# Optimization experiments

Hardware: AMD Instinct MI355X
Metric: run time of the kernel (lower is better)

Reference implementation:

```python
import jax, jax.numpy as jnp
import numpy as np

B, N, M = 262144, 8, 8      # batch, state dim, control dim (n_vars == n_controls)
H1, H21, H22 = 64, 32, 32
R2 = 16.0                   # barrier h(x) = R2 - ||x||^2
UMIN, UMAX = -1.0, 1.0


def setup_inputs() -> dict:
    key = jax.random.key(0)
    ks = jax.random.split(key, 12)
    init = lambda k, sh: jax.random.normal(k, sh, jnp.float32) / np.float32(np.sqrt(sh[0]))
    return {
        "x":   jax.random.normal(ks[0], (B, N), jnp.float32),
        "W1":  init(ks[1], (N, H1)),   "b1":  jnp.zeros((H1,), jnp.float32),
        "W21": init(ks[2], (H1, H21)), "b21": jnp.zeros((H21,), jnp.float32),
        "W22": init(ks[3], (H1, H22)), "b22": jnp.zeros((H22,), jnp.float32),
        "W31": init(ks[4], (H21, M)),  "b31": jnp.zeros((M,), jnp.float32),
        "W32": init(ks[5], (H22, 1)),  "b32": jnp.zeros((1,), jnp.float32),
        "A":   0.1 * jax.random.normal(ks[6], (N, N), jnp.float32),  # f(x) = A x
        "G":   init(ks[7], (N, M)),                                  # g(x) = G
        "mean": jnp.zeros((N,), jnp.float32),
        "std":  jnp.ones((N,), jnp.float32),
    }


def _qp_solve(p, g, c0):
    """Batched exact solution of: argmin_u 1/2||u||^2 + p.u
    s.t. UMIN <= u <= UMAX,  c0 + g . u >= 0   (one QP per row).
    KKT: u(lam) = clip(-p + lam*g, UMIN, UMAX), lam >= 0 dual of the CBF
    constraint; c(lam) = c0 + g.u(lam) is nondecreasing in lam, so lam* is
    found by bracketing + bisection, then refined in closed form on the
    frozen active set (this also yields exact implicit KKT derivatives)."""
    def c_of(lam):
        u = jnp.clip(-p + lam[:, None] * g, UMIN, UMAX)
        return c0 + jnp.sum(g * u, axis=-1)

    # bracket lambda* in [0, hi]
    hi = jax.lax.fori_loop(0, 40, lambda i, h: jnp.where(c_of(h) < 0, 2.0 * h, h),
                           jnp.ones_like(c0))

    def bis(i, lh):
        lo, hi = lh
        mid = 0.5 * (lo + hi)
        neg = c_of(mid) < 0
        return jnp.where(neg, mid, lo), jnp.where(neg, hi, mid)

    lo, hi = jax.lax.fori_loop(0, 60, bis, (jnp.zeros_like(c0), hi))
    lam_b = 0.5 * (lo + hi)

    # frozen active sets -> closed-form lambda consistent with KKT
    u_raw = -p + lam_b[:, None] * g
    low = jax.lax.stop_gradient(u_raw <= UMIN)
    high = jax.lax.stop_gradient(u_raw >= UMAX)
    free = ~(low | high)
    viol = jax.lax.stop_gradient(c_of(jnp.zeros_like(c0)) < 0)  # constraint active?
    denom = jnp.sum(jnp.where(free, g * g, 0.0), axis=-1)
    num = c0 + jnp.sum(jnp.where(low, UMIN * g, 0.0)
                       + jnp.where(high, UMAX * g, 0.0)
                       - jnp.where(free, g * p, 0.0), axis=-1)
    lam = jnp.where(viol, -num / (denom + 1e-12), 0.0)
    return jnp.where(low, UMIN, jnp.where(high, UMAX, -p + lam[:, None] * g))


def reference(x, W1, b1, W21, b21, W22, b22, W31, b31, W32, b32, A, G, mean, std):
    x0 = x * std + mean                                   # un-normalized state (B, N)
    h1 = jax.nn.relu(x @ W1 + b1)                         # (B, H1)
    x21 = jax.nn.relu(h1 @ W21 + b21)                     # (B, H21)
    x22 = jax.nn.relu(h1 @ W22 + b22)                     # (B, H22)
    px = x21 @ W31 + b31                                  # nominal control (B, M)
    alphax = 4.0 * jax.nn.sigmoid(x22 @ W32 + b32)        # class-K gain (B, 1)
    hx = R2 - jnp.sum(x0 * x0, axis=-1, keepdims=True)    # barrier value (B, 1)
    dhdx = -2.0 * x0                                      # barrier gradient (B, N)
    fxv = x0 @ A.T                                        # f(x) = A x        (B, N)
    Lfhx = jnp.sum(dhdx * fxv, axis=-1)                   # (B,)
    Lghx = dhdx @ G                                       # (B, M)
    c0 = Lfhx + (alphax * hx)[:, 0]                       # (B,)
    return _qp_solve(px, Lghx, c0)                        # safe control u (B, M)
```

## Files before the change

### kernel.cpp

```cpp
#include <hip/hip_runtime.h>

#define NN 8
#define MM 8
#define NH1 64
#define NH2 32

#define FOR8(OP) OP(0) OP(1) OP(2) OP(3) OP(4) OP(5) OP(6) OP(7)

typedef float v2f  __attribute__((ext_vector_type(2)));
typedef float sf16 __attribute__((ext_vector_type(16)));

#define S_ISSUE2(d0, d1, base, imm)                                    \
    asm volatile("s_load_dwordx16 %0, %2, %c3\n\t"                     \
                 "s_load_dwordx16 %1, %2, %c4"                         \
                 : "=&s"(d0), "=&s"(d1)                                \
                 : "s"(base), "n"(imm), "n"((imm) + 64))

#define S_ISSUE1(d0, base, imm)                                        \
    asm volatile("s_load_dwordx16 %0, %1, %c2"                         \
                 : "=&s"(d0) : "s"(base), "n"(imm))

#define S_WAIT2(d0, d1)                                                \
    asm volatile("s_waitcnt lgkmcnt(0)" : "+s"(d0), "+s"(d1))

#define S_WAIT1(d0)                                                    \
    asm volatile("s_waitcnt lgkmcnt(0)" : "+s"(d0))

#define PKFMA(acc, w, xi)                                              \
    asm("v_pk_fma_f32 %0, %1, %2, %0" : "+v"(acc) : "s"(w), "v"(xi))

__device__ __forceinline__ void compute_row(
    int row,
    const float* __restrict__ x_g,
    const float* __restrict__ W1,  const float* __restrict__ b1,
    const float* __restrict__ W21, const float* __restrict__ b21,
    const float* __restrict__ W22, const float* __restrict__ b22,
    const float* __restrict__ W31, const float* __restrict__ b31,
    const float* __restrict__ W32, const float* __restrict__ b32,
    const float* __restrict__ Amat, const float* __restrict__ Gmat,
    const float* __restrict__ mean, const float* __restrict__ std_,
    float* __restrict__ out)
{
    float x[NN];
    {
        const float4* xv = reinterpret_cast<const float4*>(x_g + (size_t)row * NN);
        float4 a0 = xv[0], a1 = xv[1];
        x[0] = a0.x; x[1] = a0.y; x[2] = a0.z; x[3] = a0.w;
        x[4] = a1.x; x[5] = a1.y; x[6] = a1.z; x[7] = a1.w;
    }

    float x0[NN];
    {
        const float4 sd0 = ((const float4*)std_)[0], sd1 = ((const float4*)std_)[1];
        const float4 mn0 = ((const float4*)mean)[0], mn1 = ((const float4*)mean)[1];
        x0[0] = fmaf(x[0], sd0.x, mn0.x); x0[1] = fmaf(x[1], sd0.y, mn0.y);
        x0[2] = fmaf(x[2], sd0.z, mn0.z); x0[3] = fmaf(x[3], sd0.w, mn0.w);
        x0[4] = fmaf(x[4], sd1.x, mn1.x); x0[5] = fmaf(x[5], sd1.y, mn1.y);
        x0[6] = fmaf(x[6], sd1.z, mn1.z); x0[7] = fmaf(x[7], sd1.w, mn1.w);
    }

    v2f hv[NH1 / 2];
#pragma unroll
    for (int j2 = 0; j2 < NH1 / 2; ++j2) hv[j2] = *(const v2f*)(b1 + 2 * j2);

    {
        sf16 rA0, rA1, rB0, rB1;
        S_ISSUE2(rA0, rA1, W1, 0);
        S_WAIT2(rA0, rA1);
#pragma unroll
        for (int u = 0; u < 16; ++u) {
            const int i = u >> 1, hh = u & 1;
            const v2f xi = { x[i], x[i] };
            if ((u & 1) == 0) {
                if (u + 1 < 16) S_ISSUE2(rB0, rB1, W1, (u + 1) * 128);
#pragma unroll
                for (int j2 = 0; j2 < 8; ++j2) { const v2f w = { rA0[2*j2], rA0[2*j2+1] }; PKFMA(hv[hh*16 + j2], w, xi); }
#pragma unroll
                for (int j2 = 0; j2 < 8; ++j2) { const v2f w = { rA1[2*j2], rA1[2*j2+1] }; PKFMA(hv[hh*16 + 8 + j2], w, xi); }
                if (u + 1 < 16) S_WAIT2(rB0, rB1);
            } else {
                if (u + 1 < 16) S_ISSUE2(rA0, rA1, W1, (u + 1) * 128);
#pragma unroll
                for (int j2 = 0; j2 < 8; ++j2) { const v2f w = { rB0[2*j2], rB0[2*j2+1] }; PKFMA(hv[hh*16 + j2], w, xi); }
#pragma unroll
                for (int j2 = 0; j2 < 8; ++j2) { const v2f w = { rB1[2*j2], rB1[2*j2+1] }; PKFMA(hv[hh*16 + 8 + j2], w, xi); }
                if (u + 1 < 16) S_WAIT2(rA0, rA1);
            }
        }
    }
    {
        const v2f zero2 = { 0.0f, 0.0f };
#pragma unroll
        for (int j2 = 0; j2 < NH1 / 2; ++j2) hv[j2] = __builtin_elementwise_max(hv[j2], zero2);
    }

    v2f a21[NH2 / 2], a22[NH2 / 2];
#pragma unroll
    for (int j2 = 0; j2 < NH2 / 2; ++j2) {
        a21[j2] = *(const v2f*)(b21 + 2 * j2);
        a22[j2] = *(const v2f*)(b22 + 2 * j2);
    }

#define L2PASS(ACC, WBASE)                                                     \
    {                                                                          \
        sf16 qA0, qA1, qB0, qB1;                                               \
        S_ISSUE2(qA0, qA1, WBASE, 0);                                          \
        S_WAIT2(qA0, qA1);                                                     \
        _Pragma("unroll")                                                      \
        for (int k = 0; k < NH1; ++k) {                                        \
            const v2f hb = (k & 1) ? hv[k >> 1].yy : hv[k >> 1].xx;            \
            if ((k & 1) == 0) {                                                \
                if (k + 1 < NH1) S_ISSUE2(qB0, qB1, WBASE, (k + 1) * 128);     \
                _Pragma("unroll")                                              \
                for (int j2 = 0; j2 < 8; ++j2) { const v2f w = { qA0[2*j2], qA0[2*j2+1] }; PKFMA(ACC[j2], w, hb); } \
                _Pragma("unroll")                                              \
                for (int j2 = 0; j2 < 8; ++j2) { const v2f w = { qA1[2*j2], qA1[2*j2+1] }; PKFMA(ACC[8 + j2], w, hb); } \
                if (k + 1 < NH1) S_WAIT2(qB0, qB1);                            \
            } else {                                                           \
                if (k + 1 < NH1) S_ISSUE2(qA0, qA1, WBASE, (k + 1) * 128);     \
                _Pragma("unroll")                                              \
                for (int j2 = 0; j2 < 8; ++j2) { const v2f w = { qB0[2*j2], qB0[2*j2+1] }; PKFMA(ACC[j2], w, hb); } \
                _Pragma("unroll")                                              \
                for (int j2 = 0; j2 < 8; ++j2) { const v2f w = { qB1[2*j2], qB1[2*j2+1] }; PKFMA(ACC[8 + j2], w, hb); } \
                if (k + 1 < NH1) S_WAIT2(qA0, qA1);                            \
            }                                                                  \
        }                                                                      \
    }

    L2PASS(a21, W21)
    L2PASS(a22, W22)
#undef L2PASS

    {
        const v2f zero2 = { 0.0f, 0.0f };
#pragma unroll
        for (int j2 = 0; j2 < NH2 / 2; ++j2) {
            a21[j2] = __builtin_elementwise_max(a21[j2], zero2);
            a22[j2] = __builtin_elementwise_max(a22[j2], zero2);
        }
    }

    sf16 wA0, wA1;
    S_ISSUE2(wA0, wA1, W32, 0);

    v2f pv[MM / 2];
#pragma unroll
    for (int j2 = 0; j2 < MM / 2; ++j2) pv[j2] = *(const v2f*)(b31 + 2 * j2);
    {
        sf16 pA, pB;
        S_ISSUE1(pA, W31, 0);
        S_WAIT1(pA);
#pragma unroll
        for (int k2 = 0; k2 < NH2 / 2; ++k2) {
            const v2f ha = a21[k2].xx, hb2 = a21[k2].yy;
            if ((k2 & 1) == 0) {
                if (k2 + 1 < 16) S_ISSUE1(pB, W31, (k2 + 1) * 64);
#pragma unroll
                for (int j2 = 0; j2 < 4; ++j2) { const v2f w = { pA[2*j2], pA[2*j2+1] }; PKFMA(pv[j2], w, ha); }
#pragma unroll
                for (int j2 = 0; j2 < 4; ++j2) { const v2f w = { pA[8 + 2*j2], pA[8 + 2*j2+1] }; PKFMA(pv[j2], w, hb2); }
                if (k2 + 1 < 16) S_WAIT1(pB);
            } else {
                if (k2 + 1 < 16) S_ISSUE1(pA, W31, (k2 + 1) * 64);
#pragma unroll
                for (int j2 = 0; j2 < 4; ++j2) { const v2f w = { pB[2*j2], pB[2*j2+1] }; PKFMA(pv[j2], w, ha); }
#pragma unroll
                for (int j2 = 0; j2 < 4; ++j2) { const v2f w = { pB[8 + 2*j2], pB[8 + 2*j2+1] }; PKFMA(pv[j2], w, hb2); }
                if (k2 + 1 < 16) S_WAIT1(pA);
            }
        }
    }

    S_WAIT2(wA0, wA1);
    float s = b32[0];
#pragma unroll
    for (int k = 0; k < 16; ++k)
        s = fmaf((k & 1) ? a22[k >> 1].y : a22[k >> 1].x, wA0[k], s);
#pragma unroll
    for (int k = 16; k < 32; ++k)
        s = fmaf((k & 1) ? a22[k >> 1].y : a22[k >> 1].x, wA1[k - 16], s);
    const float alphax = 4.0f / (1.0f + __expf(-s));

    float hx = 16.0f;
#pragma unroll
    for (int i = 0; i < NN; ++i) hx = fmaf(-x0[i], x0[i], hx);

    float dh[NN];
#pragma unroll
    for (int i = 0; i < NN; ++i) dh[i] = -2.0f * x0[i];

    float Lfhx = 0.0f;
#pragma unroll
    for (int i = 0; i < NN; ++i) {
        const float4 aq0 = *(const float4*)(Amat + i * NN);
        const float4 aq1 = *(const float4*)(Amat + i * NN + 4);
        float fx = 0.0f;
        fx = fmaf(aq0.x, x0[0], fx); fx = fmaf(aq0.y, x0[1], fx);
        fx = fmaf(aq0.z, x0[2], fx); fx = fmaf(aq0.w, x0[3], fx);
        fx = fmaf(aq1.x, x0[4], fx); fx = fmaf(aq1.y, x0[5], fx);
        fx = fmaf(aq1.z, x0[6], fx); fx = fmaf(aq1.w, x0[7], fx);
        Lfhx = fmaf(dh[i], fx, Lfhx);
    }

#define GDECL(j) float g##j = 0.0f;
    FOR8(GDECL)
#undef GDECL
#pragma unroll
    for (int i = 0; i < NN; ++i) {
        const float4 gq0 = *(const float4*)(Gmat + i * MM);
        const float4 gq1 = *(const float4*)(Gmat + i * MM + 4);
        const float da = dh[i];
        g0 = fmaf(da, gq0.x, g0); g1 = fmaf(da, gq0.y, g1);
        g2 = fmaf(da, gq0.z, g2); g3 = fmaf(da, gq0.w, g3);
        g4 = fmaf(da, gq1.x, g4); g5 = fmaf(da, gq1.y, g5);
        g6 = fmaf(da, gq1.z, g6); g7 = fmaf(da, gq1.w, g7);
    }

    const float c0 = fmaf(alphax, hx, Lfhx);

#define DECL_PG(j) const float p##j = (j & 1) ? pv[j >> 1].y : pv[j >> 1].x;
    FOR8(DECL_PG)
#undef DECL_PG

    auto c_of = [&](float lam) -> float {
        float c = c0;
#define CTERM(j) { float u = fmaf(lam, g##j, -p##j);                  \
                   u = fminf(fmaxf(u, -1.0f), 1.0f);                  \
                   c = fmaf(g##j, u, c); }
        FOR8(CTERM)
#undef CTERM
        return c;
    };

    const bool viol = (c_of(0.0f) < 0.0f);

    const float BIGR = 3.0e38f;
    float lamL = 0.0f, lamR = BIGR;
#define BP(j) {                                                        \
        const float rg = __builtin_amdgcn_rcpf(g##j);                  \
        const float bpa = (p##j - 1.0f) * rg;                          \
        const float bpb = (p##j + 1.0f) * rg;                          \
        const float ca = c_of(bpa);                                    \
        const float cb = c_of(bpb);                                    \
        lamL = (bpa > 0.0f && ca <  0.0f && bpa > lamL) ? bpa : lamL;  \
        lamR = (bpa > 0.0f && ca >= 0.0f && bpa < lamR) ? bpa : lamR;  \
        lamL = (bpb > 0.0f && cb <  0.0f && bpb > lamL) ? bpb : lamL;  \
        lamR = (bpb > 0.0f && cb >= 0.0f && bpb < lamR) ? bpb : lamR;  \
    }
    FOR8(BP)
#undef BP

    const bool infeas = (lamR == BIGR);
    float lam_t = infeas ? 1.099511627776e12f : 0.5f * (lamL + lamR);
    lam_t = viol ? lam_t : 0.0f;

    float denom = 0.0f, num = c0;
#define ASET(j)                                                        \
    const float ur##j = fmaf(lam_t, g##j, -p##j);                      \
    const bool lo##j = (ur##j <= -1.0f);                               \
    const bool hi##j = (ur##j >=  1.0f);                               \
    denom += (!(lo##j || hi##j)) ? g##j * g##j : 0.0f;                 \
    num   += lo##j ? -g##j : (hi##j ? g##j : -g##j * p##j);
    FOR8(ASET)
#undef ASET

    const float lam = viol ? (-num / (denom + 1e-12f)) : 0.0f;

#define UOUT(j) const float uo##j =                                    \
    lo##j ? -1.0f : (hi##j ? 1.0f : fmaf(lam, g##j, -p##j));
    FOR8(UOUT)
#undef UOUT

    float4* ov = reinterpret_cast<float4*>(out + (size_t)row * MM);
    ov[0] = make_float4(uo0, uo1, uo2, uo3);
    ov[1] = make_float4(uo4, uo5, uo6, uo7);
}

#define ARGS_DECL                                                       \
    const float* __restrict__ x_g,                                      \
    const float* __restrict__ W1,  const float* __restrict__ b1,        \
    const float* __restrict__ W21, const float* __restrict__ b21,       \
    const float* __restrict__ W22, const float* __restrict__ b22,       \
    const float* __restrict__ W31, const float* __restrict__ b31,       \
    const float* __restrict__ W32, const float* __restrict__ b32,       \
    const float* __restrict__ Amat, const float* __restrict__ Gmat,     \
    const float* __restrict__ mean, const float* __restrict__ std_,    \
    float* __restrict__ out
#define ARGS_PASS x_g, W1, b1, W21, b21, W22, b22, W31, b31, W32, b32, \
                  Amat, Gmat, mean, std_, out

__global__ __launch_bounds__(256, 2) void barrier_policy_clean(ARGS_DECL)
{
    const int row = blockIdx.x * 256 + threadIdx.x;
    compute_row(row, ARGS_PASS);
}

__global__ __launch_bounds__(256, 2) void barrier_policy_guard(ARGS_DECL, int B)
{
    const int row = blockIdx.x * 256 + threadIdx.x;
    if (row < B) compute_row(row, ARGS_PASS);
}

extern "C" void kernel_launch(void* const* d_in, const int* in_sizes, int n_in,
                              void* d_out, int out_size, void* d_ws, size_t ws_size,
                              hipStream_t stream) {
    const float* x    = (const float*)d_in[0];
    const float* W1   = (const float*)d_in[1];
    const float* b1   = (const float*)d_in[2];
    const float* W21  = (const float*)d_in[3];
    const float* b21  = (const float*)d_in[4];
    const float* W22  = (const float*)d_in[5];
    const float* b22  = (const float*)d_in[6];
    const float* W31  = (const float*)d_in[7];
    const float* b31  = (const float*)d_in[8];
    const float* W32  = (const float*)d_in[9];
    const float* b32  = (const float*)d_in[10];
    const float* Amat = (const float*)d_in[11];
    const float* Gmat = (const float*)d_in[12];
    const float* mean = (const float*)d_in[13];
    const float* std_ = (const float*)d_in[14];
    float* out = (float*)d_out;

    const int B = in_sizes[0] / NN;
    if (B % 256 == 0) {
        barrier_policy_clean<<<B / 256, 256, 0, stream>>>(
            x, W1, b1, W21, b21, W22, b22, W31, b31, W32, b32,
            Amat, Gmat, mean, std_, out);
    } else {
        barrier_policy_guard<<<(B + 255) / 256, 256, 0, stream>>>(
            x, W1, b1, W21, b21, W22, b22, W31, b31, W32, b32,
            Amat, Gmat, mean, std_, out, B);
    }
}
```

Measured before the change: 43.57 us.

## Compute W21 hidden layer with packed fp16 dot2 and raise occupancy bound

Adds a small prep kernel that converts W21 to packed fp16 pairs in the workspace. The main kernel packs the first hidden activations into fp16 and computes the second-layer x21 branch with v_dot2_f32_f16, which accumulates pairs along the reduction dimension in fp32. It also moves the alpha (sigmoid) computation earlier so the W32 load overlaps the ReLU, and changes launch_bounds from 2 to 4 waves per SIMD. This adds an extra launch, reduces precision of the nominal control feeding the QP, and the tighter register budget may cause spills.

```diff
diff --git a/kernel.cpp b/kernel.cpp
--- a/kernel.cpp
+++ b/kernel.cpp
@@ -1,4 +1,5 @@
 #include <hip/hip_runtime.h>
+#include <hip/hip_fp16.h>
 
 #define NN 8
 #define MM 8
@@ -9,6 +10,7 @@
 
 typedef float v2f  __attribute__((ext_vector_type(2)));
 typedef float sf16 __attribute__((ext_vector_type(16)));
+typedef __fp16 h2f __attribute__((ext_vector_type(2)));
 
 #define S_ISSUE2(d0, d1, base, imm)                                    \
     asm volatile("s_load_dwordx16 %0, %2, %c3\n\t"                     \
@@ -29,12 +31,27 @@
 #define PKFMA(acc, w, xi)                                              \
     asm("v_pk_fma_f32 %0, %1, %2, %0" : "+v"(acc) : "s"(w), "v"(xi))
 
+#define DOT2(acc, w, hp)                                               \
+    asm("v_dot2_f32_f16 %0, %2, %1, %0" : "+v"(acc) : "s"(w), "v"(hp))
+
+__global__ void prep_f16(const float* __restrict__ W21,
+                         unsigned int* __restrict__ ws)
+{
+    const int t = blockIdx.x * 256 + threadIdx.x;
+    const int k2 = t >> 5, j = t & 31;
+    const float lo = W21[(2 * k2) * NH2 + j];
+    const float hi = W21[(2 * k2 + 1) * NH2 + j];
+    const __half hlo = __float2half(lo), hhi = __float2half(hi);
+    ws[t] = ((unsigned int)__half_as_ushort(hhi) << 16) | __half_as_ushort(hlo);
+}
+
 __device__ __forceinline__ void compute_row(
     int row,
     const float* __restrict__ x_g,
     const float* __restrict__ W1,  const float* __restrict__ b1,
-    const float* __restrict__ W21, const float* __restrict__ b21,
-    const float* __restrict__ W22, const float* __restrict__ b22,
+    const float* __restrict__ ws21,
+    const float* __restrict__ b21, const float* __restrict__ b22,
+    const float* __restrict__ W22,
     const float* __restrict__ W31, const float* __restrict__ b31,
     const float* __restrict__ W32, const float* __restrict__ b32,
     const float* __restrict__ Amat, const float* __restrict__ Gmat,
@@ -94,54 +111,91 @@
         for (int j2 = 0; j2 < NH1 / 2; ++j2) hv[j2] = __builtin_elementwise_max(hv[j2], zero2);
     }
 
-    v2f a21[NH2 / 2], a22[NH2 / 2];
-#pragma unroll
-    for (int j2 = 0; j2 < NH2 / 2; ++j2) {
-        a21[j2] = *(const v2f*)(b21 + 2 * j2);
-        a22[j2] = *(const v2f*)(b22 + 2 * j2);
-    }
-
-#define L2PASS(ACC, WBASE)                                                     \
-    {                                                                          \
-        sf16 qA0, qA1, qB0, qB1;                                               \
-        S_ISSUE2(qA0, qA1, WBASE, 0);                                          \
-        S_WAIT2(qA0, qA1);                                                     \
-        _Pragma("unroll")                                                      \
-        for (int k = 0; k < NH1; ++k) {                                        \
-            const v2f hb = (k & 1) ? hv[k >> 1].yy : hv[k >> 1].xx;            \
-            if ((k & 1) == 0) {                                                \
-                if (k + 1 < NH1) S_ISSUE2(qB0, qB1, WBASE, (k + 1) * 128);     \
-                _Pragma("unroll")                                              \
-                for (int j2 = 0; j2 < 8; ++j2) { const v2f w = { qA0[2*j2], qA0[2*j2+1] }; PKFMA(ACC[j2], w, hb); } \
-                _Pragma("unroll")                                              \
-                for (int j2 = 0; j2 < 8; ++j2) { const v2f w = { qA1[2*j2], qA1[2*j2+1] }; PKFMA(ACC[8 + j2], w, hb); } \
-                if (k + 1 < NH1) S_WAIT2(qB0, qB1);                            \
-            } else {                                                           \
-                if (k + 1 < NH1) S_ISSUE2(qA0, qA1, WBASE, (k + 1) * 128);     \
-                _Pragma("unroll")                                              \
-                for (int j2 = 0; j2 < 8; ++j2) { const v2f w = { qB0[2*j2], qB0[2*j2+1] }; PKFMA(ACC[j2], w, hb); } \
-                _Pragma("unroll")                                              \
-                for (int j2 = 0; j2 < 8; ++j2) { const v2f w = { qB1[2*j2], qB1[2*j2+1] }; PKFMA(ACC[8 + j2], w, hb); } \
-                if (k + 1 < NH1) S_WAIT2(qA0, qA1);                            \
-            }                                                                  \
-        }                                                                      \
-    }
-
-    L2PASS(a21, W21)
-    L2PASS(a22, W22)
-#undef L2PASS
-
-    {
-        const v2f zero2 = { 0.0f, 0.0f };
-#pragma unroll
-        for (int j2 = 0; j2 < NH2 / 2; ++j2) {
-            a21[j2] = __builtin_elementwise_max(a21[j2], zero2);
-            a22[j2] = __builtin_elementwise_max(a22[j2], zero2);
+    v2f a22[NH2 / 2];
+#pragma unroll
+    for (int j2 = 0; j2 < NH2 / 2; ++j2) a22[j2] = *(const v2f*)(b22 + 2 * j2);
+    {
+        sf16 qA0, qA1, qB0, qB1;
+        S_ISSUE2(qA0, qA1, W22, 0);
+        S_WAIT2(qA0, qA1);
+#pragma unroll
+        for (int k = 0; k < NH1; ++k) {
+            const v2f hb = (k & 1) ? hv[k >> 1].yy : hv[k >> 1].xx;
+            if ((k & 1) == 0) {
+                if (k + 1 < NH1) S_ISSUE2(qB0, qB1, W22, (k + 1) * 128);
+#pragma unroll
+                for (int j2 = 0; j2 < 8; ++j2) { const v2f w = { qA0[2*j2], qA0[2*j2+1] }; PKFMA(a22[j2], w, hb); }
+#pragma unroll
+                for (int j2 = 0; j2 < 8; ++j2) { const v2f w = { qA1[2*j2], qA1[2*j2+1] }; PKFMA(a22[8 + j2], w, hb); }
+                if (k + 1 < NH1) S_WAIT2(qB0, qB1);
+            } else {
+                if (k + 1 < NH1) S_ISSUE2(qA0, qA1, W22, (k + 1) * 128);
+#pragma unroll
+                for (int j2 = 0; j2 < 8; ++j2) { const v2f w = { qB0[2*j2], qB0[2*j2+1] }; PKFMA(a22[j2], w, hb); }
+#pragma unroll
+                for (int j2 = 0; j2 < 8; ++j2) { const v2f w = { qB1[2*j2], qB1[2*j2+1] }; PKFMA(a22[8 + j2], w, hb); }
+                if (k + 1 < NH1) S_WAIT2(qA0, qA1);
+            }
         }
     }
 
     sf16 wA0, wA1;
     S_ISSUE2(wA0, wA1, W32, 0);
+    {
+        const v2f zero2 = { 0.0f, 0.0f };
+#pragma unroll
+        for (int j2 = 0; j2 < NH2 / 2; ++j2) a22[j2] = __builtin_elementwise_max(a22[j2], zero2);
+    }
+    S_WAIT2(wA0, wA1);
+    float s = b32[0];
+#pragma unroll
+    for (int k = 0; k < 16; ++k)
+        s = fmaf((k & 1) ? a22[k >> 1].y : a22[k >> 1].x, wA0[k], s);
+#pragma unroll
+    for (int k = 16; k < 32; ++k)
+        s = fmaf((k & 1) ? a22[k >> 1].y : a22[k >> 1].x, wA1[k - 16], s);
+    const float alphax = 4.0f / (1.0f + __expf(-s));
+
+    float hpk[NH1 / 2];
+#pragma unroll
+    for (int k2 = 0; k2 < NH1 / 2; ++k2) {
+        h2f hp = __builtin_amdgcn_cvt_pkrtz(hv[k2].x, hv[k2].y);
+        hpk[k2] = __builtin_bit_cast(float, hp);
+    }
+
+    float a21s[NH2];
+#pragma unroll
+    for (int j4 = 0; j4 < NH2 / 4; ++j4) {
+        const float4 i21 = ((const float4*)b21)[j4];
+        a21s[4*j4]   = i21.x; a21s[4*j4+1] = i21.y;
+        a21s[4*j4+2] = i21.z; a21s[4*j4+3] = i21.w;
+    }
+    {
+        sf16 A0, A1, B0, B1;
+        S_ISSUE2(A0, A1, ws21, 0);
+        S_WAIT2(A0, A1);
+#pragma unroll
+        for (int k2 = 0; k2 < 32; ++k2) {
+            const float hp = hpk[k2];
+            if ((k2 & 1) == 0) {
+                if (k2 + 1 < 32) S_ISSUE2(B0, B1, ws21, (k2 + 1) * 128);
+#pragma unroll
+                for (int j = 0; j < 16; ++j) DOT2(a21s[j],      A0[j], hp);
+#pragma unroll
+                for (int j = 0; j < 16; ++j) DOT2(a21s[16 + j], A1[j], hp);
+                if (k2 + 1 < 32) S_WAIT2(B0, B1);
+            } else {
+                if (k2 + 1 < 32) S_ISSUE2(A0, A1, ws21, (k2 + 1) * 128);
+#pragma unroll
+                for (int j = 0; j < 16; ++j) DOT2(a21s[j],      B0[j], hp);
+#pragma unroll
+                for (int j = 0; j < 16; ++j) DOT2(a21s[16 + j], B1[j], hp);
+                if (k2 + 1 < 32) S_WAIT2(A0, A1);
+            }
+        }
+    }
+#pragma unroll
+    for (int j = 0; j < NH2; ++j) a21s[j] = fmaxf(a21s[j], 0.0f);
 
     v2f pv[MM / 2];
 #pragma unroll
@@ -152,7 +206,8 @@
         S_WAIT1(pA);
 #pragma unroll
         for (int k2 = 0; k2 < NH2 / 2; ++k2) {
-            const v2f ha = a21[k2].xx, hb2 = a21[k2].yy;
+            const v2f ha  = { a21s[2*k2],     a21s[2*k2]     };
+            const v2f hb2 = { a21s[2*k2 + 1], a21s[2*k2 + 1] };
             if ((k2 & 1) == 0) {
                 if (k2 + 1 < 16) S_ISSUE1(pB, W31, (k2 + 1) * 64);
 #pragma unroll
@@ -170,16 +225,6 @@
             }
         }
     }
-
-    S_WAIT2(wA0, wA1);
-    float s = b32[0];
-#pragma unroll
-    for (int k = 0; k < 16; ++k)
-        s = fmaf((k & 1) ? a22[k >> 1].y : a22[k >> 1].x, wA0[k], s);
-#pragma unroll
-    for (int k = 16; k < 32; ++k)
-        s = fmaf((k & 1) ? a22[k >> 1].y : a22[k >> 1].x, wA1[k - 16], s);
-    const float alphax = 4.0f / (1.0f + __expf(-s));
 
     float hx = 16.0f;
 #pragma unroll
@@ -279,23 +324,24 @@
 #define ARGS_DECL                                                       \
     const float* __restrict__ x_g,                                      \
     const float* __restrict__ W1,  const float* __restrict__ b1,        \
-    const float* __restrict__ W21, const float* __restrict__ b21,       \
-    const float* __restrict__ W22, const float* __restrict__ b22,       \
+    const float* __restrict__ ws21,                                     \
+    const float* __restrict__ b21, const float* __restrict__ b22,       \
+    const float* __restrict__ W22,                                      \
     const float* __restrict__ W31, const float* __restrict__ b31,       \
     const float* __restrict__ W32, const float* __restrict__ b32,       \
     const float* __restrict__ Amat, const float* __restrict__ Gmat,     \
     const float* __restrict__ mean, const float* __restrict__ std_,    \
     float* __restrict__ out
-#define ARGS_PASS x_g, W1, b1, W21, b21, W22, b22, W31, b31, W32, b32, \
+#define ARGS_PASS x_g, W1, b1, ws21, b21, b22, W22, W31, b31, W32, b32, \
                   Amat, Gmat, mean, std_, out
 
-__global__ __launch_bounds__(256, 2) void barrier_policy_clean(ARGS_DECL)
+__global__ __launch_bounds__(256, 4) void barrier_policy_clean(ARGS_DECL)
 {
     const int row = blockIdx.x * 256 + threadIdx.x;
     compute_row(row, ARGS_PASS);
 }
 
-__global__ __launch_bounds__(256, 2) void barrier_policy_guard(ARGS_DECL, int B)
+__global__ __launch_bounds__(256, 4) void barrier_policy_guard(ARGS_DECL, int B)
 {
     const int row = blockIdx.x * 256 + threadIdx.x;
     if (row < B) compute_row(row, ARGS_PASS);
@@ -321,14 +367,17 @@
     const float* std_ = (const float*)d_in[14];
     float* out = (float*)d_out;
 
+    prep_f16<<<4, 256, 0, stream>>>(W21, (unsigned int*)d_ws);
+    const float* ws21 = (const float*)d_ws;
+
     const int B = in_sizes[0] / NN;
     if (B % 256 == 0) {
         barrier_policy_clean<<<B / 256, 256, 0, stream>>>(
-            x, W1, b1, W21, b21, W22, b22, W31, b31, W32, b32,
+            x, W1, b1, ws21, b21, b22, W22, W31, b31, W32, b32,
             Amat, Gmat, mean, std_, out);
     } else {
         barrier_policy_guard<<<(B + 255) / 256, 256, 0, stream>>>(
-            x, W1, b1, W21, b21, W22, b22, W31, b31, W32, b32,
+            x, W1, b1, ws21, b21, b22, W22, W31, b31, W32, b32,
             Amat, Gmat, mean, std_, out, B);
     }
 }
```

Result: slower. 44.66 us (+2.5%).
